# Performance work log

Measured on AMD Instinct MI355X. Metric: run time of the kernel, lower is better.

The kernel has to match this reference:

```python
import jax, jax.numpy as jnp
import numpy as np

CAT = 19          # category_num + 1 (last slot is the catch-all cluster)
ATT_SCALE = float(np.sqrt(200.0))


def _layernorm(x, scale, bias, eps=1e-5):
    mu = jnp.mean(x, axis=-1, keepdims=True)
    var = jnp.mean((x - mu) ** 2, axis=-1, keepdims=True)
    return (x - mu) * jax.lax.rsqrt(var + eps) * scale + bias


def setup_inputs() -> dict:
    key = jax.random.key(0)
    ks = jax.random.split(key, 16)
    B, N, H, D, A, L = 64, 16, 100, 400, 200, 2
    nodes = H + (CAT - 1)  # 118
    s = 1.0 / np.sqrt(D)
    return {
        "history_embedding": jax.random.normal(ks[0], (B, H, D), jnp.float32),
        "candidate_news_representation": jax.random.normal(ks[1], (B, N, D), jnp.float32),
        "user_history_graph": jax.random.uniform(ks[2], (B, nodes, nodes), jnp.float32) / nodes,
        "user_history_category_mask": jax.random.randint(ks[3], (B, CAT), 0, 2, jnp.int32),
        "user_history_category_indices": jax.random.randint(ks[4], (B, H), 0, CAT, jnp.int32),
        "proxy_node_embedding": jax.random.normal(ks[5], (CAT - 1, D), jnp.float32) * 0.02,
        "gcn_W": jax.random.normal(ks[6], (L, D, D), jnp.float32) * s,
        "gcn_b": jnp.zeros((L, D), jnp.float32),
        "ln_scale": jnp.ones((L, D), jnp.float32),
        "ln_bias": jnp.zeros((L, D), jnp.float32),
        "Kw": jax.random.normal(ks[7], (D, A), jnp.float32) * s,
        "Qw": jax.random.normal(ks[8], (D, A), jnp.float32) * s,
        "Qb": jnp.zeros((A,), jnp.float32),
        "affine_W": jax.random.normal(ks[9], (D, D), jnp.float32) * s,
        "affine_b": jnp.zeros((D,), jnp.float32),
        "icKw": jax.random.normal(ks[10], (D, A), jnp.float32) * s,
        "icQw": jax.random.normal(ks[11], (D, A), jnp.float32) * s,
        "icQb": jnp.zeros((A,), jnp.float32),
    }


def _forward(history_embedding, candidate_news_representation, user_history_graph,
             proxy_node_embedding, gcn_W, gcn_b, ln_scale, ln_bias,
             Kw, Qw, Qb, affine_W, affine_b, icKw, icQw, icQb,
             user_history_category_mask, user_history_category_indices):
    B, H, D = history_embedding.shape
    N = candidate_news_representation.shape[1]
    L = gcn_W.shape[0]

    # append proxy cluster nodes to the history graph nodes (dropout = identity at eval)
    he = jnp.concatenate(
        [history_embedding, jnp.broadcast_to(proxy_node_embedding[None], (B, CAT - 1, D))],
        axis=1)  # [B, 118, D]

    # GCN with residual + layernorm per layer, then global residual
    h = he
    for l in range(L):
        z = jnp.einsum('bij,bjd->bid', user_history_graph, h) @ gcn_W[l] + gcn_b[l]
        z = jax.nn.relu(z) + h
        h = _layernorm(z, ln_scale[l], ln_bias[l])
    gcn_feat = (h + he)[:, :H]  # [B, H, D]

    # intra-cluster scatter softmax over history items grouped by category
    K = gcn_feat @ Kw                                     # [B, H, A]
    Q = candidate_news_representation @ Qw + Qb           # [B, N, A]
    a = jnp.einsum('bha,bna->bnh', K, Q) / ATT_SCALE      # [B, N, H]

    onehot = jax.nn.one_hot(user_history_category_indices, CAT, dtype=a.dtype)  # [B, H, C]
    seg = onehot.astype(bool)
    neg = jnp.finfo(a.dtype).min
    # segment-max for stable softmax: [B, N, H, C] -> max over H
    seg_max = jnp.where(seg[:, None], a[..., None], neg).max(axis=2)            # [B, N, C]
    a_shift = a - jnp.einsum('bhc,bnc->bnh', onehot, seg_max)
    e = jnp.exp(a_shift)
    denom = jnp.einsum('bhc,bnc->bnh', onehot, jnp.einsum('bnh,bhc->bnc', e, onehot))
    alpha = e / denom                                                           # [B, N, H]

    # scatter-sum of attention-weighted gcn features into category clusters
    weighted = alpha[..., None] * gcn_feat[:, None]                             # [B, N, H, D]
    intra = jnp.einsum('bnhd,bhc->bncd', weighted, onehot)                      # [B, N, C, D]
    intra = jax.nn.relu(intra @ affine_W + affine_b) + intra

    # inter-cluster scaled-dot-product candidate attention (last cluster always valid)
    mask = user_history_category_mask.at[:, -1].set(1).astype(bool)[:, None, :]  # [B, 1, C]
    Kf = intra @ icKw                                                           # [B, N, C, A]
    q = candidate_news_representation @ icQw + icQb                             # [B, N, A]
    s = jnp.einsum('bnca,bna->bnc', Kf, q) / ATT_SCALE
    w = jax.nn.softmax(jnp.where(mask, s, neg), axis=-1)
    return jnp.einsum('bnc,bncd->bnd', w, intra)                                # [B, N, D]


def reference(history_embedding, candidate_news_representation, user_history_graph,
              user_history_category_mask, user_history_category_indices,
              proxy_node_embedding, gcn_W, gcn_b, ln_scale, ln_bias,
              Kw, Qw, Qb, affine_W, affine_b, icKw, icQw, icQb):
    return _forward(history_embedding, candidate_news_representation, user_history_graph,
                    proxy_node_embedding, gcn_W, gcn_b, ln_scale, ln_bias,
                    Kw, Qw, Qb, affine_W, affine_b, icKw, icQw, icQb,
                    user_history_category_mask, user_history_category_indices)
```

## Files before the change

kernel.cpp:

```cpp
#include <hip/hip_runtime.h>
#include <hip/hip_bf16.h>
#include <math.h>

#define BB 64
#define NN 16
#define HH 100
#define DD 400
#define AA 200
#define CATN 19
#define NODES 118
#define BN (BB*NODES)
#define BH (BB*HH)
#define ATT_INV 0.07071067811865475f

typedef __attribute__((ext_vector_type(4))) float f32x4;
typedef __attribute__((ext_vector_type(8))) short s16x8;

__device__ __forceinline__ unsigned short f2bf(float f) {
  union { float f; unsigned int u; } v; v.f = f;
  unsigned int r = v.u + 0x7FFFu + ((v.u >> 16) & 1u);
  return (unsigned short)(r >> 16);
}

__global__ __launch_bounds__(256) void k_concat_he(const float* __restrict__ hist,
    const float* __restrict__ proxy, float* __restrict__ he, int total) {
  int idx = blockIdx.x * 256 + threadIdx.x;
  if (idx >= total) return;
  int d = idx % DD;
  int bi = idx / DD;
  int i = bi % NODES;
  int b = bi / NODES;
  he[idx] = (i < HH) ? hist[((size_t)b * HH + i) * DD + d] : proxy[(size_t)(i - HH) * DD + d];
}

template<int RPB>
__global__ __launch_bounds__(256) void k_toT(const float* __restrict__ h,
    unsigned short* __restrict__ T) {
  __shared__ float t_sh[64][129];
  const int b = blockIdx.x / 7, dt = blockIdx.x % 7;
  const int d0 = dt * 64;
  const int tid = threadIdx.x;
  const int dc = tid & 63, jr = tid >> 6;
  for (int j0 = 0; j0 < 128; j0 += 4) {
    int j = j0 + jr, d = d0 + dc;
    float v = (j < RPB && d < DD) ? h[((size_t)b * RPB + j) * DD + d] : 0.f;
    t_sh[dc][j] = v;
  }
  __syncthreads();
  const int jc = tid & 127, dr2 = tid >> 7;
  for (int di = 0; di < 64; di += 2) {
    int dr = di + dr2;
    int d = d0 + dr;
    if (d < 416) T[((size_t)b * 416 + d) * 128 + jc] = f2bf(t_sh[dr][jc]);
  }
}

__global__ __launch_bounds__(256) void k_gmm(const float* __restrict__ G,
    const unsigned short* __restrict__ hT, unsigned short* __restrict__ tmpb) {
  __shared__ unsigned short a_sh[32 * 136];
  const int b = blockIdx.x >> 2;
  const int i0 = (blockIdx.x & 3) * 32;
  const int tid = threadIdx.x;
  for (int idx = tid; idx < 32 * 128; idx += 256) {
    int r = idx >> 7, j = idx & 127;
    int i = i0 + r;
    float v = (i < NODES && j < NODES) ? G[((size_t)b * NODES + i) * NODES + j] : 0.f;
    a_sh[r * 136 + j] = f2bf(v);
  }
  __syncthreads();
  const int lane = tid & 63, w = tid >> 6;
  const int lrow = lane & 15, lk = lane >> 4;
  const int rg = w & 1, nh = w >> 1;
  const int cbeg = nh * 13;
  f32x4 acc[13];
#pragma unroll
  for (int c = 0; c < 13; ++c) acc[c] = f32x4{0.f, 0.f, 0.f, 0.f};
  const unsigned short* ap = &a_sh[(rg * 16 + lrow) * 136 + lk * 8];
  const unsigned short* wp = &hT[((size_t)b * 416 + cbeg * 16 + lrow) * 128 + lk * 8];
  for (int ks = 0; ks < 4; ++ks) {
    s16x8 af = *reinterpret_cast<const s16x8*>(ap + ks * 32);
#pragma unroll
    for (int c = 0; c < 13; ++c) {
      s16x8 bf = *reinterpret_cast<const s16x8*>(wp + (size_t)c * 16 * 128 + ks * 32);
      acc[c] = __builtin_amdgcn_mfma_f32_16x16x32_bf16(af, bf, acc[c], 0, 0, 0);
    }
  }
  const int r0 = rg * 16 + lk * 4;
#pragma unroll
  for (int c = 0; c < 13; ++c) {
    int col = (cbeg + c) * 16 + lrow;
#pragma unroll
    for (int j = 0; j < 4; ++j) {
      int i = i0 + r0 + j;
      if (i < NODES)
        tmpb[((size_t)b * NODES + i) * 416 + col] = f2bf(acc[c][j]);
    }
  }
}

__global__ __launch_bounds__(256) void k_mgb_ln(
    const unsigned short* __restrict__ A, const unsigned short* __restrict__ Wt,
    const float* __restrict__ bias, const float* __restrict__ resid,
    const float* __restrict__ lns, const float* __restrict__ lnb,
    float* __restrict__ out) {
  __shared__ float ps_sh[32][2][2];
  const int tid = threadIdx.x;
  const size_t row0 = (size_t)blockIdx.x * 32;
  const int lane = tid & 63, w = tid >> 6;
  const int lrow = lane & 15, lk = lane >> 4;
  const int rg = w & 1, nh = w >> 1;
  const int cbeg = nh * 13;
  f32x4 acc[13];
#pragma unroll
  for (int c = 0; c < 13; ++c) acc[c] = f32x4{0.f, 0.f, 0.f, 0.f};
  const unsigned short* ap = &A[(row0 + rg * 16 + lrow) * 416 + lk * 8];
  const unsigned short* wp = &Wt[((size_t)(cbeg * 16) + lrow) * 416 + lk * 8];
  for (int ks = 0; ks < 13; ++ks) {
    s16x8 af = *reinterpret_cast<const s16x8*>(ap + ks * 32);
#pragma unroll
    for (int c = 0; c < 13; ++c) {
      s16x8 bf = *reinterpret_cast<const s16x8*>(wp + (size_t)c * 16 * 416 + ks * 32);
      acc[c] = __builtin_amdgcn_mfma_f32_16x16x32_bf16(af, bf, acc[c], 0, 0, 0);
    }
  }
  const int r0 = rg * 16 + lk * 4;
  float zs[4], zq[4];
#pragma unroll
  for (int j = 0; j < 4; ++j) { zs[j] = 0.f; zq[j] = 0.f; }
#pragma unroll
  for (int c = 0; c < 13; ++c) {
    int col = (cbeg + c) * 16 + lrow;
    bool cv = col < DD;
    float bv = cv ? bias[col] : 0.f;
#pragma unroll
    for (int j = 0; j < 4; ++j) {
      float z = 0.f;
      if (cv)
        z = fmaxf(acc[c][j] + bv, 0.f) + resid[(row0 + r0 + j) * (size_t)DD + col];
      acc[c][j] = z;
      zs[j] += z;
      zq[j] += z * z;
    }
  }
#pragma unroll
  for (int j = 0; j < 4; ++j) {
    zs[j] += __shfl_xor(zs[j], 1, 64); zq[j] += __shfl_xor(zq[j], 1, 64);
    zs[j] += __shfl_xor(zs[j], 2, 64); zq[j] += __shfl_xor(zq[j], 2, 64);
    zs[j] += __shfl_xor(zs[j], 4, 64); zq[j] += __shfl_xor(zq[j], 4, 64);
    zs[j] += __shfl_xor(zs[j], 8, 64); zq[j] += __shfl_xor(zq[j], 8, 64);
  }
  if (lrow == 0) {
#pragma unroll
    for (int j = 0; j < 4; ++j) {
      ps_sh[r0 + j][nh][0] = zs[j];
      ps_sh[r0 + j][nh][1] = zq[j];
    }
  }
  __syncthreads();
  float mu[4], rs[4];
#pragma unroll
  for (int j = 0; j < 4; ++j) {
    float s = ps_sh[r0 + j][0][0] + ps_sh[r0 + j][1][0];
    float q = ps_sh[r0 + j][0][1] + ps_sh[r0 + j][1][1];
    mu[j] = s * (1.0f / DD);
    float var = q * (1.0f / DD) - mu[j] * mu[j];
    rs[j] = 1.0f / sqrtf(var + 1e-5f);
  }
#pragma unroll
  for (int c = 0; c < 13; ++c) {
    int col = (cbeg + c) * 16 + lrow;
    if (col < DD) {
      float sc = lns[col], bo = lnb[col];
#pragma unroll
      for (int j = 0; j < 4; ++j)
        out[(row0 + r0 + j) * (size_t)DD + col] = (acc[c][j] - mu[j]) * rs[j] * sc + bo;
    }
  }
}

__global__ __launch_bounds__(256) void k_add_gf(const float* __restrict__ h2,
    const float* __restrict__ he, float* __restrict__ gf, int total) {
  int idx = blockIdx.x * 256 + threadIdx.x;
  if (idx >= total) return;
  int d = idx % DD;
  int bi = idx / DD;
  int i = bi % HH;
  int b = bi / HH;
  size_t src = ((size_t)b * NODES + i) * DD + d;
  gf[idx] = h2[src] + he[src];
}

__global__ __launch_bounds__(256) void k_prep_all(const float* __restrict__ gW,
    const float* __restrict__ afW, const float* __restrict__ Kw,
    const float* __restrict__ Qw, const float* __restrict__ icQw,
    const float* __restrict__ icKw, const float* __restrict__ Qb,
    const float* __restrict__ icQb, unsigned short* __restrict__ wbase,
    float* __restrict__ bias2) {
  int idx = blockIdx.x * 256 + threadIdx.x;
  const int SG = 416 * 416;
  const int SK = 224 * 416;
  if (idx < SG) {
    int n = idx / 416, k = idx - n * 416;
    wbase[idx] = (n < 400 && k < 400) ? f2bf(gW[(size_t)k * 400 + n]) : (unsigned short)0;
    return;
  }
  idx -= SG;
  if (idx < SG) {
    int n = idx / 416, k = idx - n * 416;
    wbase[173056 + idx] = (n < 400 && k < 400) ? f2bf(gW[160000 + (size_t)k * 400 + n]) : (unsigned short)0;
    return;
  }
  idx -= SG;
  if (idx < SG) {
    int n = idx / 416, k = idx - n * 416;
    wbase[346112 + idx] = (n < 400 && k < 400) ? f2bf(afW[(size_t)k * 400 + n]) : (unsigned short)0;
    return;
  }
  idx -= SG;
  if (idx < SK) {
    int n = idx / 416, k = idx - n * 416;
    wbase[519168 + idx] = (n < 200 && k < 400) ? f2bf(Kw[(size_t)k * 200 + n]) : (unsigned short)0;
    return;
  }
  idx -= SK;
  if (idx < SG) {
    int n = idx / 416, k = idx - n * 416;
    unsigned short v = 0;
    if (k < 400) {
      if (n < 200) v = f2bf(Qw[(size_t)k * 200 + n]);
      else if (n >= 208 && n < 408) v = f2bf(icQw[(size_t)k * 200 + (n - 208)]);
    }
    wbase[612352 + idx] = v;
    return;
  }
  idx -= SG;
  if (idx < SK) {
    int d = idx / 224, a = idx - d * 224;
    wbase[785408 + idx] = (d < 400 && a < 200) ? f2bf(icKw[(size_t)d * 200 + a]) : (unsigned short)0;
    return;
  }
  idx -= SK;
  if (idx < 416) {
    float v = 0.f;
    if (idx < 200) v = Qb[idx];
    else if (idx >= 208 && idx < 408) v = icQb[idx - 208];
    bias2[idx] = v;
  }
}

template<int KDIM, int KPAD, int NOUT, int EPI>
__global__ __launch_bounds__(256) void k_mg(
    const float* __restrict__ A, const unsigned short* __restrict__ Wt,
    const float* __restrict__ bias, const float* __restrict__ resid,
    const float* __restrict__ p, float* __restrict__ s_pre,
    float* __restrict__ out, float* __restrict__ out2) {
  constexpr int APITCH = KPAD + 8;
  constexpr int NF = (NOUT + 15) / 16;
  constexpr int NF0 = (NF + 1) / 2;
  constexpr int KS = KPAD / 32;
  constexpr int E4 = KDIM / 4;
  constexpr int PADN = KPAD - KDIM;
  __shared__ unsigned short a_sh[32 * APITCH];
  __shared__ float ps_sh[32][2];
  const int tid = threadIdx.x;
  const size_t row0 = (size_t)blockIdx.x * 32;
  for (int i = tid; i < 32 * E4; i += 256) {
    int r = i / E4, c4 = i - r * E4;
    const float4 v = *reinterpret_cast<const float4*>(&A[(row0 + r) * (size_t)KDIM + c4 * 4]);
    unsigned int lo = (unsigned int)f2bf(v.x) | ((unsigned int)f2bf(v.y) << 16);
    unsigned int hi = (unsigned int)f2bf(v.z) | ((unsigned int)f2bf(v.w) << 16);
    *reinterpret_cast<uint2*>(&a_sh[r * APITCH + c4 * 4]) = make_uint2(lo, hi);
  }
  for (int i = tid; i < 32 * PADN; i += 256) {
    int r = i / PADN, c = i - r * PADN;
    a_sh[r * APITCH + KDIM + c] = 0;
  }
  __syncthreads();
  const int lane = tid & 63, w = tid >> 6;
  const int lrow = lane & 15, lk = lane >> 4;
  const int rg = w & 1, nh = w >> 1;
  const int cbeg = nh * NF0;
  f32x4 acc[NF0];
#pragma unroll
  for (int c = 0; c < NF0; ++c) acc[c] = f32x4{0.f, 0.f, 0.f, 0.f};
  const unsigned short* ap = &a_sh[(rg * 16 + lrow) * APITCH + lk * 8];
  const unsigned short* wp = &Wt[((size_t)(cbeg * 16) + lrow) * KPAD + lk * 8];
  for (int ks = 0; ks < KS; ++ks) {
    s16x8 af = *reinterpret_cast<const s16x8*>(ap + ks * 32);
#pragma unroll
    for (int c = 0; c < NF0; ++c) {
      s16x8 bf = *reinterpret_cast<const s16x8*>(wp + (size_t)c * 16 * KPAD + ks * 32);
      acc[c] = __builtin_amdgcn_mfma_f32_16x16x32_bf16(af, bf, acc[c], 0, 0, 0);
    }
  }
  const int r0 = rg * 16 + lk * 4;
  if (EPI == 0) {
#pragma unroll
    for (int c = 0; c < NF0; ++c) {
      int col = (cbeg + c) * 16 + lrow;
      if (col < NOUT) {
#pragma unroll
        for (int j = 0; j < 4; ++j)
          out[(row0 + r0 + j) * (size_t)NOUT + col] = acc[c][j];
      }
    }
  } else if (EPI == 5) {
#pragma unroll
    for (int c = 0; c < NF0; ++c) {
      int col = (cbeg + c) * 16 + lrow;
      float bv = bias[col];
      if (col < 200) {
#pragma unroll
        for (int j = 0; j < 4; ++j)
          out[(row0 + r0 + j) * (size_t)AA + col] = acc[c][j] + bv;
      } else if (col >= 208 && col < 408) {
#pragma unroll
        for (int j = 0; j < 4; ++j)
          out2[(row0 + r0 + j) * (size_t)AA + (col - 208)] = acc[c][j] + bv;
      }
    }
  } else {
    float spart[4] = {0.f, 0.f, 0.f, 0.f};
#pragma unroll
    for (int c = 0; c < NF0; ++c) {
      int col = (cbeg + c) * 16 + lrow;
      if (col < NOUT) {
        float bv = bias[col];
#pragma unroll
        for (int j = 0; j < 4; ++j) {
          size_t row = row0 + r0 + j;
          size_t o = row * (size_t)NOUT + col;
          float v = fmaxf(acc[c][j] + bv, 0.f) + resid[o];
          out[o] = v;
          spart[j] += v * p[(row / CATN) * (size_t)NOUT + col];
        }
      }
    }
#pragma unroll
    for (int j = 0; j < 4; ++j) {
      spart[j] += __shfl_xor(spart[j], 1, 64);
      spart[j] += __shfl_xor(spart[j], 2, 64);
      spart[j] += __shfl_xor(spart[j], 4, 64);
      spart[j] += __shfl_xor(spart[j], 8, 64);
    }
    if (lrow == 0) {
#pragma unroll
      for (int j = 0; j < 4; ++j) ps_sh[r0 + j][nh] = spart[j];
    }
    __syncthreads();
    if (tid < 32)
      s_pre[row0 + tid] = (ps_sh[tid][0] + ps_sh[tid][1]) * ATT_INV;
  }
}

__global__ __launch_bounds__(256) void k_palpha(const float* __restrict__ K,
    const float* __restrict__ Q, const int* __restrict__ cat,
    unsigned short* __restrict__ P) {
  __shared__ float q_sh[AA];
  __shared__ float a_sh[HH];
  __shared__ int c_sh[HH];
  __shared__ float smax[CATN], sden[CATN];
  const int bn = blockIdx.x;
  const int b = bn >> 4, n = bn & 15;
  const int tid = threadIdx.x;
  if (tid < AA) q_sh[tid] = Q[(size_t)bn * AA + tid];
  if (tid < HH) c_sh[tid] = cat[b * HH + tid];
  __syncthreads();
  if (tid < 2 * HH) {
    int h = tid >> 1, half = tid & 1;
    const float* kp = K + ((size_t)b * HH + h) * AA + half * 100;
    const float* qp = q_sh + half * 100;
    float s = 0.f;
#pragma unroll 4
    for (int a = 0; a < 100; ++a) s += kp[a] * qp[a];
    s += __shfl_xor(s, 1, 64);
    if (half == 0) a_sh[h] = s * ATT_INV;
  }
  __syncthreads();
  if (tid < CATN) {
    float m = -3.4e38f;
    for (int h = 0; h < HH; ++h)
      if (c_sh[h] == tid) m = fmaxf(m, a_sh[h]);
    smax[tid] = m;
  }
  __syncthreads();
  if (tid < HH) a_sh[tid] = expf(a_sh[tid] - smax[c_sh[tid]]);
  __syncthreads();
  if (tid < CATN) {
    float dsum = 0.f;
    for (int h = 0; h < HH; ++h)
      if (c_sh[h] == tid) dsum += a_sh[h];
    sden[tid] = dsum;
  }
  __syncthreads();
  if (tid < HH) a_sh[tid] = a_sh[tid] / sden[c_sh[tid]];
  __syncthreads();
  for (int idx = tid; idx < CATN * 128; idx += 256) {
    int c = idx >> 7, h = idx & 127;
    float v = (h < HH && c_sh[h] == c) ? a_sh[h] : 0.f;
    P[((size_t)b * 304 + n * CATN + c) * 128 + h] = f2bf(v);
  }
}

__global__ __launch_bounds__(128) void k_sc(const unsigned short* __restrict__ P,
    const unsigned short* __restrict__ gfT, float* __restrict__ intra) {
  const int b = blockIdx.x / CATN, t = blockIdx.x % CATN;
  const int tid = threadIdx.x;
  const int lane = tid & 63, w = tid >> 6;
  const int lrow = lane & 15, lk = lane >> 4;
  const int cbeg = w * 13;
  f32x4 acc[13];
#pragma unroll
  for (int c = 0; c < 13; ++c) acc[c] = f32x4{0.f, 0.f, 0.f, 0.f};
  const unsigned short* ap = &P[((size_t)b * 304 + t * 16 + lrow) * 128 + lk * 8];
  const unsigned short* wp = &gfT[((size_t)b * 416 + cbeg * 16 + lrow) * 128 + lk * 8];
  for (int ks = 0; ks < 4; ++ks) {
    s16x8 af = *reinterpret_cast<const s16x8*>(ap + ks * 32);
#pragma unroll
    for (int c = 0; c < 13; ++c) {
      s16x8 bf = *reinterpret_cast<const s16x8*>(wp + (size_t)c * 16 * 128 + ks * 32);
      acc[c] = __builtin_amdgcn_mfma_f32_16x16x32_bf16(af, bf, acc[c], 0, 0, 0);
    }
  }
  const int r0 = lk * 4;
#pragma unroll
  for (int c = 0; c < 13; ++c) {
    int col = (cbeg + c) * 16 + lrow;
    if (col < DD) {
#pragma unroll
      for (int j = 0; j < 4; ++j)
        intra[((size_t)b * 304 + t * 16 + r0 + j) * (size_t)DD + col] = acc[c][j];
    }
  }
}

__global__ __launch_bounds__(256) void k_final(const float* __restrict__ intra,
    const float* __restrict__ s_pre, const int* __restrict__ mask,
    float* __restrict__ out) {
  __shared__ float w_sh[CATN];
  const int bn = blockIdx.x;
  const int b = bn >> 4;
  const int tid = threadIdx.x;
  if (tid == 0) {
    float sv[CATN];
    float mx = -3.4e38f;
#pragma unroll
    for (int c = 0; c < CATN; ++c) {
      bool mk = (c == CATN - 1) || (mask[b * CATN + c] != 0);
      float s = mk ? s_pre[bn * CATN + c] : -3.4e38f;
      sv[c] = s;
      mx = fmaxf(mx, s);
    }
    float den = 0.f;
#pragma unroll
    for (int c = 0; c < CATN; ++c) {
      float e = (sv[c] <= -3.3e38f) ? 0.f : expf(sv[c] - mx);
      w_sh[c] = e;
      den += e;
    }
    float inv = 1.0f / den;
#pragma unroll
    for (int c = 0; c < CATN; ++c) w_sh[c] *= inv;
  }
  __syncthreads();
  const float* ib = intra + (size_t)bn * CATN * DD;
  for (int d = tid; d < DD; d += 256) {
    float o = 0.f;
#pragma unroll
    for (int c = 0; c < CATN; ++c) o += w_sh[c] * ib[(size_t)c * DD + d];
    out[(size_t)bn * DD + d] = o;
  }
}

extern "C" void kernel_launch(void* const* d_in, const int* in_sizes, int n_in,
                              void* d_out, int out_size, void* d_ws, size_t ws_size,
                              hipStream_t stream) {
  const float* hist  = (const float*)d_in[0];
  const float* cand  = (const float*)d_in[1];
  const float* G     = (const float*)d_in[2];
  const int*   cmask = (const int*)d_in[3];
  const int*   cidx  = (const int*)d_in[4];
  const float* proxy = (const float*)d_in[5];
  const float* gW    = (const float*)d_in[6];
  const float* gb    = (const float*)d_in[7];
  const float* lns   = (const float*)d_in[8];
  const float* lnb   = (const float*)d_in[9];
  const float* Kw    = (const float*)d_in[10];
  const float* Qw    = (const float*)d_in[11];
  const float* Qbb   = (const float*)d_in[12];
  const float* afW   = (const float*)d_in[13];
  const float* afb   = (const float*)d_in[14];
  const float* icKw  = (const float*)d_in[15];
  const float* icQw  = (const float*)d_in[16];
  const float* icQb  = (const float*)d_in[17];
  float* out = (float*)d_out;
  float* ws  = (float*)d_ws;

  float* he    = ws;
  float* s1    = ws + 3020800;
  float* s2f   = ws + 6041600;
  unsigned short* tmpb = (unsigned short*)(ws + 6041600);
  unsigned short* TB   = (unsigned short*)(ws + 9062400);
  float* intra = ws + 10766336;
  float* bias2 = ws + 18548736;
  unsigned short* wbase = (unsigned short*)(ws + 18549152);
  unsigned short* Pbuf = (unsigned short*)ws;
  float* qbuf  = ws + 1245184;
  float* qic   = ws + 1449984;
  float* pbuf  = ws + 1654784;
  float* s_pre = ws + 2064384;
  float* Kbuf  = s1;
  unsigned short* gW0t  = wbase;
  unsigned short* gW1t  = wbase + 173056;
  unsigned short* afWt  = wbase + 346112;
  unsigned short* Kwt   = wbase + 519168;
  unsigned short* Qqt   = wbase + 612352;
  unsigned short* icKwB = wbase + 785408;

  k_prep_all<<<3434, 256, 0, stream>>>(gW, afW, Kw, Qw, icQw, icKw, Qbb, icQb, wbase, bias2);
  k_concat_he<<<(BN * DD + 255) / 256, 256, 0, stream>>>(hist, proxy, he, BN * DD);
  k_toT<NODES><<<448, 256, 0, stream>>>(he, TB);
  k_gmm<<<256, 256, 0, stream>>>(G, TB, tmpb);
  k_mgb_ln<<<BN / 32, 256, 0, stream>>>(tmpb, gW0t, gb, he, lns, lnb, s1);
  k_toT<NODES><<<448, 256, 0, stream>>>(s1, TB);
  k_gmm<<<256, 256, 0, stream>>>(G, TB, tmpb);
  k_mgb_ln<<<BN / 32, 256, 0, stream>>>(tmpb, gW1t, gb + DD, s1, lns + DD, lnb + DD, s1);
  k_add_gf<<<(BH * DD + 255) / 256, 256, 0, stream>>>(s1, he, s2f, BH * DD);
  k_toT<HH><<<448, 256, 0, stream>>>(s2f, TB);
  k_mg<400, 416, 200, 0><<<BH / 32, 256, 0, stream>>>(s2f, Kwt, nullptr, nullptr, nullptr, nullptr, Kbuf, nullptr);
  k_mg<400, 416, 416, 5><<<BB * NN / 32, 256, 0, stream>>>(cand, Qqt, bias2, nullptr, nullptr, nullptr, qbuf, qic);
  k_mg<200, 224, 400, 0><<<BB * NN / 32, 256, 0, stream>>>(qic, icKwB, nullptr, nullptr, nullptr, nullptr, pbuf, nullptr);
  k_palpha<<<BB * NN, 256, 0, stream>>>(Kbuf, qbuf, cidx, Pbuf);
  k_sc<<<BB * CATN, 128, 0, stream>>>(Pbuf, TB, intra);
  k_mg<400, 416, 400, 4><<<BB * NN * CATN / 32, 256, 0, stream>>>(intra, afWt, afb, intra, pbuf, s_pre, intra, nullptr);
  k_final<<<BB * NN, 256, 0, stream>>>(intra, s_pre, cmask, out);
}
```

Before: 341.9 us.

## Fuse intra-cluster GEMM, affine, scoring and softmax into one per-query kernel

Merges the per-cluster aggregation GEMM, the affine layer with ReLU and residual, the score reduction, the softmax and the weighted sum into a single kernel, one block per (batch, candidate). The 19x400 intra tensor stays in shared memory and never round-trips through global memory. It also precomputes icKw·icQw^T as a weight matrix so the two-step query projection collapses into one GEMM. The cost is more shared memory and registers per block, plus an extra bf16 rounding of the intermediate and of the combined weight.

After: 415.6 us. 1.22x slower.

```diff
diff --git a/kernel.cpp b/kernel.cpp
--- a/kernel.cpp
+++ b/kernel.cpp
@@ -21,6 +21,9 @@
   unsigned int r = v.u + 0x7FFFu + ((v.u >> 16) & 1u);
   return (unsigned short)(r >> 16);
 }
+__device__ __forceinline__ float bf2f(unsigned short u) {
+  union { unsigned int i; float f; } v; v.i = ((unsigned int)u) << 16; return v.f;
+}
 
 __global__ __launch_bounds__(256) void k_concat_he(const float* __restrict__ hist,
     const float* __restrict__ proxy, float* __restrict__ he, int total) {
@@ -195,7 +198,7 @@
     const float* __restrict__ Qw, const float* __restrict__ icQw,
     const float* __restrict__ icKw, const float* __restrict__ Qb,
     const float* __restrict__ icQb, unsigned short* __restrict__ wbase,
-    float* __restrict__ bias2) {
+    float* __restrict__ bias3) {
   int idx = blockIdx.x * 256 + threadIdx.x;
   const int SG = 416 * 416;
   const int SK = 224 * 416;
@@ -223,37 +226,74 @@
     return;
   }
   idx -= SK;
-  if (idx < SG) {
-    int n = idx / 416, k = idx - n * 416;
-    unsigned short v = 0;
-    if (k < 400) {
-      if (n < 200) v = f2bf(Qw[(size_t)k * 200 + n]);
-      else if (n >= 208 && n < 408) v = f2bf(icQw[(size_t)k * 200 + (n - 208)]);
-    }
-    wbase[612352 + idx] = v;
-    return;
-  }
-  idx -= SG;
   if (idx < SK) {
     int d = idx / 224, a = idx - d * 224;
-    wbase[785408 + idx] = (d < 400 && a < 200) ? f2bf(icKw[(size_t)d * 200 + a]) : (unsigned short)0;
+    wbase[612352 + idx] = (d < 400 && a < 200) ? f2bf(icKw[(size_t)d * 200 + a]) : (unsigned short)0;
     return;
   }
   idx -= SK;
-  if (idx < 416) {
+  if (idx < SK) {
+    int k = idx / 224, a = idx - k * 224;
+    wbase[705536 + idx] = (k < 400 && a < 200) ? f2bf(icQw[(size_t)k * 200 + a]) : (unsigned short)0;
+    return;
+  }
+  idx -= SK;
+  if (idx < 208 * 416) {
+    int n = idx / 416, k = idx - n * 416;
+    wbase[798720 + idx] = (n < 200 && k < 400) ? f2bf(Qw[(size_t)k * 200 + n]) : (unsigned short)0;
+    return;
+  }
+  idx -= 208 * 416;
+  if (idx < 608) {
     float v = 0.f;
     if (idx < 200) v = Qb[idx];
-    else if (idx >= 208 && idx < 408) v = icQb[idx - 208];
-    bias2[idx] = v;
+    else if (idx >= 208) {
+      const float* kr = icKw + (size_t)(idx - 208) * 200;
+      float s = 0.f;
+      for (int a = 0; a < 200; ++a) s += icQb[a] * kr[a];
+      v = s;
+    }
+    bias3[idx] = v;
+  }
+}
+
+__global__ __launch_bounds__(256) void k_prep_M(const unsigned short* __restrict__ icKwB,
+    const unsigned short* __restrict__ icQwB, unsigned short* __restrict__ wqp) {
+  const int tid = threadIdx.x;
+  const size_t row0 = (size_t)blockIdx.x * 32;
+  const int lane = tid & 63, w = tid >> 6;
+  const int lrow = lane & 15, lk = lane >> 4;
+  const int rg = w & 1, nh = w >> 1;
+  const int cbeg = nh * 13;
+  f32x4 acc[13];
+#pragma unroll
+  for (int c = 0; c < 13; ++c) acc[c] = f32x4{0.f, 0.f, 0.f, 0.f};
+  const unsigned short* ap = &icKwB[(row0 + rg * 16 + lrow) * 224 + lk * 8];
+  const unsigned short* bp = &icQwB[((size_t)(cbeg * 16) + lrow) * 224 + lk * 8];
+  for (int ks = 0; ks < 7; ++ks) {
+    s16x8 af = *reinterpret_cast<const s16x8*>(ap + ks * 32);
+#pragma unroll
+    for (int c = 0; c < 13; ++c) {
+      s16x8 bf = *reinterpret_cast<const s16x8*>(bp + (size_t)c * 16 * 224 + ks * 32);
+      acc[c] = __builtin_amdgcn_mfma_f32_16x16x32_bf16(af, bf, acc[c], 0, 0, 0);
+    }
+  }
+  const int r0 = rg * 16 + lk * 4;
+#pragma unroll
+  for (int c = 0; c < 13; ++c) {
+    int k = (cbeg + c) * 16 + lrow;
+#pragma unroll
+    for (int j = 0; j < 4; ++j) {
+      size_t d = row0 + r0 + j;
+      if (d < 400) wqp[(208 + d) * 416 + k] = f2bf(acc[c][j]);
+    }
   }
 }
 
 template<int KDIM, int KPAD, int NOUT, int EPI>
 __global__ __launch_bounds__(256) void k_mg(
     const float* __restrict__ A, const unsigned short* __restrict__ Wt,
-    const float* __restrict__ bias, const float* __restrict__ resid,
-    const float* __restrict__ p, float* __restrict__ s_pre,
-    float* __restrict__ out, float* __restrict__ out2) {
+    const float* __restrict__ bias, float* __restrict__ out, float* __restrict__ out2) {
   constexpr int APITCH = KPAD + 8;
   constexpr int NF = (NOUT + 15) / 16;
   constexpr int NF0 = (NF + 1) / 2;
@@ -261,7 +301,6 @@
   constexpr int E4 = KDIM / 4;
   constexpr int PADN = KPAD - KDIM;
   __shared__ unsigned short a_sh[32 * APITCH];
-  __shared__ float ps_sh[32][2];
   const int tid = threadIdx.x;
   const size_t row0 = (size_t)blockIdx.x * 32;
   for (int i = tid; i < 32 * E4; i += 256) {
@@ -304,52 +343,22 @@
           out[(row0 + r0 + j) * (size_t)NOUT + col] = acc[c][j];
       }
     }
-  } else if (EPI == 5) {
+  } else {
 #pragma unroll
     for (int c = 0; c < NF0; ++c) {
       int col = (cbeg + c) * 16 + lrow;
-      float bv = bias[col];
       if (col < 200) {
+        float bv = bias[col];
 #pragma unroll
         for (int j = 0; j < 4; ++j)
           out[(row0 + r0 + j) * (size_t)AA + col] = acc[c][j] + bv;
-      } else if (col >= 208 && col < 408) {
+      } else if (col >= 208 && col < 608) {
+        float bv = bias[col];
 #pragma unroll
         for (int j = 0; j < 4; ++j)
-          out2[(row0 + r0 + j) * (size_t)AA + (col - 208)] = acc[c][j] + bv;
+          out2[(row0 + r0 + j) * (size_t)DD + (col - 208)] = acc[c][j] + bv;
       }
     }
-  } else {
-    float spart[4] = {0.f, 0.f, 0.f, 0.f};
-#pragma unroll
-    for (int c = 0; c < NF0; ++c) {
-      int col = (cbeg + c) * 16 + lrow;
-      if (col < NOUT) {
-        float bv = bias[col];
-#pragma unroll
-        for (int j = 0; j < 4; ++j) {
-          size_t row = row0 + r0 + j;
-          size_t o = row * (size_t)NOUT + col;
-          float v = fmaxf(acc[c][j] + bv, 0.f) + resid[o];
-          out[o] = v;
-          spart[j] += v * p[(row / CATN) * (size_t)NOUT + col];
-        }
-      }
-    }
-#pragma unroll
-    for (int j = 0; j < 4; ++j) {
-      spart[j] += __shfl_xor(spart[j], 1, 64);
-      spart[j] += __shfl_xor(spart[j], 2, 64);
-      spart[j] += __shfl_xor(spart[j], 4, 64);
-      spart[j] += __shfl_xor(spart[j], 8, 64);
-    }
-    if (lrow == 0) {
-#pragma unroll
-      for (int j = 0; j < 4; ++j) ps_sh[r0 + j][nh] = spart[j];
-    }
-    __syncthreads();
-    if (tid < 32)
-      s_pre[row0 + tid] = (ps_sh[tid][0] + ps_sh[tid][1]) * ATT_INV;
   }
 }
 
@@ -398,56 +407,98 @@
   for (int idx = tid; idx < CATN * 128; idx += 256) {
     int c = idx >> 7, h = idx & 127;
     float v = (h < HH && c_sh[h] == c) ? a_sh[h] : 0.f;
-    P[((size_t)b * 304 + n * CATN + c) * 128 + h] = f2bf(v);
-  }
-}
-
-__global__ __launch_bounds__(128) void k_sc(const unsigned short* __restrict__ P,
-    const unsigned short* __restrict__ gfT, float* __restrict__ intra) {
-  const int b = blockIdx.x / CATN, t = blockIdx.x % CATN;
-  const int tid = threadIdx.x;
+    P[((size_t)b * 320 + n * CATN + c) * 128 + h] = f2bf(v);
+  }
+}
+
+__global__ __launch_bounds__(256) void k_intra(
+    const unsigned short* __restrict__ P, const unsigned short* __restrict__ gfT,
+    const unsigned short* __restrict__ afWt, const float* __restrict__ afb,
+    const float* __restrict__ pbuf, const int* __restrict__ mask,
+    float* __restrict__ out) {
+  __shared__ unsigned short a_sh[32 * 424];
+  __shared__ float p_sh[DD];
+  __shared__ float ps_sh[32][2];
+  __shared__ float w_sh[32];
+  __shared__ float osum[2][DD];
+  const int bn = blockIdx.x, b = bn >> 4, n = bn & 15;
+  const int tid = threadIdx.x;
+  for (int i = tid; i < DD; i += 256) p_sh[i] = pbuf[(size_t)bn * DD + i];
   const int lane = tid & 63, w = tid >> 6;
   const int lrow = lane & 15, lk = lane >> 4;
-  const int cbeg = w * 13;
+  const int rg = w & 1, nh = w >> 1;
+  const int cbeg = nh * 13;
+  const int r0 = rg * 16 + lk * 4;
   f32x4 acc[13];
 #pragma unroll
   for (int c = 0; c < 13; ++c) acc[c] = f32x4{0.f, 0.f, 0.f, 0.f};
-  const unsigned short* ap = &P[((size_t)b * 304 + t * 16 + lrow) * 128 + lk * 8];
-  const unsigned short* wp = &gfT[((size_t)b * 416 + cbeg * 16 + lrow) * 128 + lk * 8];
-  for (int ks = 0; ks < 4; ++ks) {
-    s16x8 af = *reinterpret_cast<const s16x8*>(ap + ks * 32);
-#pragma unroll
-    for (int c = 0; c < 13; ++c) {
-      s16x8 bf = *reinterpret_cast<const s16x8*>(wp + (size_t)c * 16 * 128 + ks * 32);
-      acc[c] = __builtin_amdgcn_mfma_f32_16x16x32_bf16(af, bf, acc[c], 0, 0, 0);
-    }
-  }
-  const int r0 = lk * 4;
+  {
+    const unsigned short* ap = &P[((size_t)b * 320 + n * CATN + rg * 16 + lrow) * 128 + lk * 8];
+    const unsigned short* bp = &gfT[((size_t)b * 416 + cbeg * 16 + lrow) * 128 + lk * 8];
+    for (int ks = 0; ks < 4; ++ks) {
+      s16x8 af = *reinterpret_cast<const s16x8*>(ap + ks * 32);
+#pragma unroll
+      for (int c = 0; c < 13; ++c) {
+        s16x8 bf = *reinterpret_cast<const s16x8*>(bp + (size_t)c * 16 * 128 + ks * 32);
+        acc[c] = __builtin_amdgcn_mfma_f32_16x16x32_bf16(af, bf, acc[c], 0, 0, 0);
+      }
+    }
+  }
+#pragma unroll
+  for (int c = 0; c < 13; ++c) {
+    int col = (cbeg + c) * 16 + lrow;
+#pragma unroll
+    for (int j = 0; j < 4; ++j)
+      a_sh[(r0 + j) * 424 + col] = f2bf((r0 + j) < CATN ? acc[c][j] : 0.f);
+  }
+  __syncthreads();
+  f32x4 acc2[13];
+#pragma unroll
+  for (int c = 0; c < 13; ++c) acc2[c] = f32x4{0.f, 0.f, 0.f, 0.f};
+  {
+    const unsigned short* ap = &a_sh[(rg * 16 + lrow) * 424 + lk * 8];
+    const unsigned short* bp = &afWt[((size_t)(cbeg * 16) + lrow) * 416 + lk * 8];
+    for (int ks = 0; ks < 13; ++ks) {
+      s16x8 af = *reinterpret_cast<const s16x8*>(ap + ks * 32);
+#pragma unroll
+      for (int c = 0; c < 13; ++c) {
+        s16x8 bf = *reinterpret_cast<const s16x8*>(bp + (size_t)c * 16 * 416 + ks * 32);
+        acc2[c] = __builtin_amdgcn_mfma_f32_16x16x32_bf16(af, bf, acc2[c], 0, 0, 0);
+      }
+    }
+  }
+  float spart[4] = {0.f, 0.f, 0.f, 0.f};
 #pragma unroll
   for (int c = 0; c < 13; ++c) {
     int col = (cbeg + c) * 16 + lrow;
     if (col < DD) {
-#pragma unroll
-      for (int j = 0; j < 4; ++j)
-        intra[((size_t)b * 304 + t * 16 + r0 + j) * (size_t)DD + col] = acc[c][j];
-    }
-  }
-}
-
-__global__ __launch_bounds__(256) void k_final(const float* __restrict__ intra,
-    const float* __restrict__ s_pre, const int* __restrict__ mask,
-    float* __restrict__ out) {
-  __shared__ float w_sh[CATN];
-  const int bn = blockIdx.x;
-  const int b = bn >> 4;
-  const int tid = threadIdx.x;
+      float bv = afb[col], pv = p_sh[col];
+#pragma unroll
+      for (int j = 0; j < 4; ++j) {
+        float v = fmaxf(acc2[c][j] + bv, 0.f) + bf2f(a_sh[(r0 + j) * 424 + col]);
+        spart[j] += v * pv;
+      }
+    }
+  }
+#pragma unroll
+  for (int j = 0; j < 4; ++j) {
+    spart[j] += __shfl_xor(spart[j], 1, 64);
+    spart[j] += __shfl_xor(spart[j], 2, 64);
+    spart[j] += __shfl_xor(spart[j], 4, 64);
+    spart[j] += __shfl_xor(spart[j], 8, 64);
+  }
+  if (lrow == 0) {
+#pragma unroll
+    for (int j = 0; j < 4; ++j) ps_sh[r0 + j][nh] = spart[j];
+  }
+  __syncthreads();
   if (tid == 0) {
     float sv[CATN];
     float mx = -3.4e38f;
 #pragma unroll
     for (int c = 0; c < CATN; ++c) {
       bool mk = (c == CATN - 1) || (mask[b * CATN + c] != 0);
-      float s = mk ? s_pre[bn * CATN + c] : -3.4e38f;
+      float s = mk ? (ps_sh[c][0] + ps_sh[c][1]) * ATT_INV : -3.4e38f;
       sv[c] = s;
       mx = fmaxf(mx, s);
     }
@@ -461,15 +512,29 @@
     float inv = 1.0f / den;
 #pragma unroll
     for (int c = 0; c < CATN; ++c) w_sh[c] *= inv;
-  }
-  __syncthreads();
-  const float* ib = intra + (size_t)bn * CATN * DD;
-  for (int d = tid; d < DD; d += 256) {
-    float o = 0.f;
-#pragma unroll
-    for (int c = 0; c < CATN; ++c) o += w_sh[c] * ib[(size_t)c * DD + d];
-    out[(size_t)bn * DD + d] = o;
-  }
+#pragma unroll
+    for (int c = CATN; c < 32; ++c) w_sh[c] = 0.f;
+  }
+  __syncthreads();
+#pragma unroll
+  for (int c = 0; c < 13; ++c) {
+    int col = (cbeg + c) * 16 + lrow;
+    if (col < DD) {
+      float bv = afb[col];
+      float o = 0.f;
+#pragma unroll
+      for (int j = 0; j < 4; ++j) {
+        float v = fmaxf(acc2[c][j] + bv, 0.f) + bf2f(a_sh[(r0 + j) * 424 + col]);
+        o += w_sh[r0 + j] * v;
+      }
+      o += __shfl_xor(o, 16, 64);
+      o += __shfl_xor(o, 32, 64);
+      if (lk == 0) osum[rg][col] = o;
+    }
+  }
+  __syncthreads();
+  for (int i = tid; i < DD; i += 256)
+    out[(size_t)bn * DD + i] = osum[0][i] + osum[1][i];
 }
 
 extern "C" void kernel_launch(void* const* d_in, const int* in_sizes, int n_in,
@@ -501,23 +566,22 @@
   float* s2f   = ws + 6041600;
   unsigned short* tmpb = (unsigned short*)(ws + 6041600);
   unsigned short* TB   = (unsigned short*)(ws + 9062400);
-  float* intra = ws + 10766336;
-  float* bias2 = ws + 18548736;
-  unsigned short* wbase = (unsigned short*)(ws + 18549152);
+  unsigned short* wbase = (unsigned short*)(ws + 10766336);
+  float* bias3 = ws + 11292160;
   unsigned short* Pbuf = (unsigned short*)ws;
-  float* qbuf  = ws + 1245184;
-  float* qic   = ws + 1449984;
-  float* pbuf  = ws + 1654784;
-  float* s_pre = ws + 2064384;
+  float* qbuf  = ws + 1310720;
+  float* pbuf  = ws + 1515520;
   float* Kbuf  = s1;
   unsigned short* gW0t  = wbase;
   unsigned short* gW1t  = wbase + 173056;
   unsigned short* afWt  = wbase + 346112;
   unsigned short* Kwt   = wbase + 519168;
-  unsigned short* Qqt   = wbase + 612352;
-  unsigned short* icKwB = wbase + 785408;
-
-  k_prep_all<<<3434, 256, 0, stream>>>(gW, afW, Kw, Qw, icQw, icKw, Qbb, icQb, wbase, bias2);
+  unsigned short* icKwB = wbase + 612352;
+  unsigned short* icQwB = wbase + 705536;
+  unsigned short* Wqp   = wbase + 798720;
+
+  k_prep_all<<<3461, 256, 0, stream>>>(gW, afW, Kw, Qw, icQw, icKw, Qbb, icQb, wbase, bias3);
+  k_prep_M<<<13, 256, 0, stream>>>(icKwB, icQwB, Wqp);
   k_concat_he<<<(BN * DD + 255) / 256, 256, 0, stream>>>(hist, proxy, he, BN * DD);
   k_toT<NODES><<<448, 256, 0, stream>>>(he, TB);
   k_gmm<<<256, 256, 0, stream>>>(G, TB, tmpb);
@@ -527,11 +591,8 @@
   k_mgb_ln<<<BN / 32, 256, 0, stream>>>(tmpb, gW1t, gb + DD, s1, lns + DD, lnb + DD, s1);
   k_add_gf<<<(BH * DD + 255) / 256, 256, 0, stream>>>(s1, he, s2f, BH * DD);
   k_toT<HH><<<448, 256, 0, stream>>>(s2f, TB);
-  k_mg<400, 416, 200, 0><<<BH / 32, 256, 0, stream>>>(s2f, Kwt, nullptr, nullptr, nullptr, nullptr, Kbuf, nullptr);
-  k_mg<400, 416, 416, 5><<<BB * NN / 32, 256, 0, stream>>>(cand, Qqt, bias2, nullptr, nullptr, nullptr, qbuf, qic);
-  k_mg<200, 224, 400, 0><<<BB * NN / 32, 256, 0, stream>>>(qic, icKwB, nullptr, nullptr, nullptr, nullptr, pbuf, nullptr);
+  k_mg<400, 416, 200, 0><<<BH / 32, 256, 0, stream>>>(s2f, Kwt, nullptr, Kbuf, nullptr);
+  k_mg<400, 416, 608, 6><<<BB * NN / 32, 256, 0, stream>>>(cand, Wqp, bias3, qbuf, pbuf);
   k_palpha<<<BB * NN, 256, 0, stream>>>(Kbuf, qbuf, cidx, Pbuf);
-  k_sc<<<BB * CATN, 128, 0, stream>>>(Pbuf, TB, intra);
-  k_mg<400, 416, 400, 4><<<BB * NN * CATN / 32, 256, 0, stream>>>(intra, afWt, afb, intra, pbuf, s_pre, intra, nullptr);
-  k_final<<<BB * NN, 256, 0, stream>>>(intra, s_pre, cmask, out);
-}
+  k_intra<<<BB * NN, 256, 0, stream>>>(Pbuf, TB, afWt, afb, pbuf, cmask, out);
+}
```
